# Performance work log

Measured on AMD Instinct MI355X. Metric: run time of the kernel, lower is better.

## Reference

```python
import jax, jax.numpy as jnp
import numpy as np

HEADS = 8
DIM_HEAD = 64
GROUPS = 32  # min(dim//4, 32) with dim=256
EPS = 1e-5

def setup_inputs() -> dict:
    key = jax.random.key(0)
    ks = jax.random.split(key, 5)
    C, H, W = 256, 256, 256
    hidden = HEADS * DIM_HEAD  # 512
    x = jax.random.normal(ks[0], (C, H, W), dtype=jnp.float32)
    gn_w = jnp.ones((C,), dtype=jnp.float32)
    gn_b = jnp.zeros((C,), dtype=jnp.float32)
    qkv_w = jax.random.normal(ks[1], (3 * hidden, C), dtype=jnp.float32) * (1.0 / np.sqrt(C))
    qkv_b = jax.random.normal(ks[2], (3 * hidden,), dtype=jnp.float32) * 0.02
    out_w = jax.random.normal(ks[3], (C, hidden), dtype=jnp.float32) * (1.0 / np.sqrt(hidden))
    out_b = jax.random.normal(ks[4], (C,), dtype=jnp.float32) * 0.02
    return {"x": x, "gn_w": gn_w, "gn_b": gn_b, "qkv_w": qkv_w,
            "qkv_b": qkv_b, "out_w": out_w, "out_b": out_b}

def reference(x, gn_w, gn_b, qkv_w, qkv_b, out_w, out_b):
    C, H, W = x.shape
    n = H * W
    # GroupNorm over (channels-in-group, h, w)
    xg = x.reshape(GROUPS, C // GROUPS, H, W)
    mean = xg.mean(axis=(1, 2, 3), keepdims=True)
    var = xg.var(axis=(1, 2, 3), keepdims=True)
    xn = ((xg - mean) * jax.lax.rsqrt(var + EPS)).reshape(C, H, W)
    xn = xn * gn_w[:, None, None] + gn_b[:, None, None]
    # 1x1 conv QKV projection
    qkv = jnp.einsum('oc,chw->ohw', qkv_w, xn) + qkv_b[:, None, None]
    # split as '(qkv heads c) h w -> qkv heads c (h w)'
    q, k, v = qkv.reshape(3, HEADS, DIM_HEAD, n)
    k = jax.nn.softmax(k, axis=-1)  # softmax over spatial axis
    context = jnp.einsum('hdn,hen->hde', k, v)   # [heads, d, d] small
    out = jnp.einsum('hde,hdn->hen', context, q)  # [heads, d, n]
    out = out.reshape(HEADS * DIM_HEAD, H, W)
    # 1x1 conv output projection
    return jnp.einsum('oc,chw->ohw', out_w, out) + out_b[:, None, None]
```

## Files before the change

kernel.cpp:

```cpp
#include <hip/hip_runtime.h>
#include <stdint.h>

typedef __attribute__((ext_vector_type(8))) short bf16x8;
typedef __attribute__((ext_vector_type(4))) float f32x4;
typedef __attribute__((ext_vector_type(4))) unsigned int u32x4;

#define NSP 65536

#define WS_XN     0ULL
#define WS_WFRAG  33554432ULL
#define WS_WEFRAG 34078720ULL
#define WS_PART   34209792ULL
#define WS_AB     34211840ULL
#define WS_CTX    34215936ULL
#define WS_W2     34347008ULL
#define WS_WEFF   35395584ULL
#define WS_BEFF   35657728ULL


__device__ __forceinline__ unsigned short f2bf(float f) {
  union { float f; uint32_t u; } v; v.f = f;
  uint32_t r = v.u + 0x7FFFu + ((v.u >> 16) & 1u);
  return (unsigned short)(r >> 16);
}
__device__ __forceinline__ float bf2f(unsigned short b) {
  union { uint32_t u; float f; } v; v.u = ((uint32_t)b) << 16;
  return v.f;
}

__global__ void k_stats(const float* __restrict__ x, float* __restrict__ part) {
  __shared__ float ss[256], sq[256];
  const int t = threadIdx.x, b = blockIdx.x;
  const f32x4* p = (const f32x4*)(x + (size_t)b * 65536);
  float s = 0.f, qq = 0.f;
  for (int k = 0; k < 64; ++k) {
    f32x4 v = __builtin_nontemporal_load(p + t + 256 * k);
    s  += v[0] + v[1] + v[2] + v[3];
    qq += v[0] * v[0] + v[1] * v[1] + v[2] * v[2] + v[3] * v[3];
  }
  ss[t] = s; sq[t] = qq;
  __syncthreads();
  for (int st = 128; st > 0; st >>= 1) {
    if (t < st) { ss[t] += ss[t + st]; sq[t] += sq[t + st]; }
    __syncthreads();
  }
  if (t == 0) { part[2 * b] = ss[0]; part[2 * b + 1] = sq[0]; }
}

__global__ void k_coef(const float* __restrict__ part, const float* __restrict__ gn_w,
                       const float* __restrict__ gn_b, float* __restrict__ ab) {
  const int c = threadIdx.x;
  const int g = c >> 3;
  float s = 0.f, q = 0.f;
  for (int j = 0; j < 8; ++j) { s += part[(g * 8 + j) * 2]; q += part[(g * 8 + j) * 2 + 1]; }
  const float inv = 1.0f / 524288.0f;
  const float mean = s * inv;
  const float var = q * inv - mean * mean;
  const float rstd = rsqrtf(var + 1e-5f);
  const float a = gn_w[c] * rstd;
  ab[c] = a;
  ab[256 + c] = gn_b[c] - mean * a;
}

__global__ void k_xn(const float* __restrict__ x, const float* __restrict__ ab,
                     unsigned short* __restrict__ xnf) {
  __shared__ float tile[64][66];
  const int t = threadIdx.x;
  const int nb = blockIdx.x, cb = blockIdx.y;
  {
    const int cl = t >> 2, nc = t & 3;
    const int c = cb * 64 + cl;
    const float a = ab[c], b = ab[256 + c];
    const f32x4* src = (const f32x4*)(x + (size_t)c * NSP + nb * 64 + nc * 16);
#pragma unroll
    for (int j = 0; j < 4; ++j) {
      f32x4 v = __builtin_nontemporal_load(src + j);
      v = v * a + b;
      *(f32x4*)&tile[cl][nc * 16 + j * 4] = v;
    }
  }
  __syncthreads();
  {
    const int l = t & 63, w0 = t >> 6;
    u32x4* xnf4 = (u32x4*)xnf;
#pragma unroll
    for (int u2 = 0; u2 < 2; ++u2) {
      const int fp = w0 + u2 * 4;
      const int fl = fp >> 1, ksl = fp & 1;
      union { unsigned short s[8]; u32x4 v; } pk2;
#pragma unroll
      for (int e = 0; e < 8; ++e)
        pk2.s[e] = f2bf(tile[ksl * 32 + (l >> 4) * 8 + e][fl * 16 + (l & 15)]);
      xnf4[((size_t)(nb * 4 + fl) * 8 + cb * 2 + ksl) * 64 + l] = pk2.v;
    }
  }
}

__global__ void k_wfrag(const float* __restrict__ qkv_w, unsigned short* __restrict__ wf) {
  const int blk = blockIdx.x;
  const int l = threadIdx.x;
  const int row = 512 + (blk & 63) * 16 + (l & 15);
  const int c0 = (blk >> 6) * 32 + (l >> 4) * 8;
  const float* src = qkv_w + (size_t)row * 256 + c0;
  union { unsigned short s[8]; u32x4 v; } u;
#pragma unroll
  for (int j = 0; j < 8; ++j) u.s[j] = f2bf(src[j]);
  *(u32x4*)(wf + ((size_t)blk * 64 + l) * 8) = u.v;
}

__launch_bounds__(512, 1)
__global__ void k_kvctx(const unsigned short* __restrict__ xnf,
                        const unsigned short* __restrict__ wfrag,
                        const float* __restrict__ qkv_b,
                        float* __restrict__ sump, float* __restrict__ ctxp) {
  __shared__ __align__(16) char lds[133120];
  const int t = threadIdx.x;
  const int w = t >> 6, l = t & 63;
  const int q = l & 15;
  const int h = blockIdx.x >> 5;
  const int chunk = blockIdx.x & 31;

  {
    const u32x4* wsrc = (const u32x4*)wfrag;
    u32x4* wdst = (u32x4*)lds;
#pragma unroll
    for (int r = 0; r < 8; ++r) {
      const int e = r * 512 + t;
      const int entry = e >> 6, l2 = e & 63;
      const int ph = entry >> 5, ks = (entry >> 2) & 7, jj = entry & 3;
      wdst[e] = wsrc[((size_t)(ks * 64 + ph * 32 + h * 4 + jj)) * 64 + l2];
    }
  }

  const f32x4 fz = {0.f, 0.f, 0.f, 0.f};
  f32x4 ctxa[4][4];
#pragma unroll
  for (int a = 0; a < 4; ++a)
#pragma unroll
    for (int b = 0; b < 4; ++b) ctxa[a][b] = fz;
  float srow[4] = {0.f, 0.f, 0.f, 0.f};
  float bk[4], bv[4];
#pragma unroll
  for (int jj = 0; jj < 4; ++jj) {
    bk[jj] = qkv_b[512 + h * 64 + jj * 16 + q];
    bv[jj] = qkv_b[1024 + h * 64 + jj * 16 + q];
  }

  const u32x4* xnf4 = (const u32x4*)xnf;
  u32x4* xa4 = (u32x4*)(lds + 65536);

  for (int st = 0; st < 8; ++st) {
    const size_t rg0 = (size_t)chunk * 128 + st * 16;
    __syncthreads();
#pragma unroll
    for (int r = 0; r < 8; ++r)
      xa4[r * 512 + t] = xnf4[rg0 * 512 + r * 512 + t];
    __syncthreads();
    const u32x4* gB = xnf4 + (rg0 + 8 + w) * 512 + l;

    f32x4 ak[2][4] = {{fz, fz, fz, fz}, {fz, fz, fz, fz}};
#pragma unroll
    for (int ks = 0; ks < 8; ++ks) {
      const bf16x8 xaA = *(const bf16x8*)(lds + 65536 + ((w * 8 + ks) * 64 + l) * 16);
      const bf16x8 xaB = *(const bf16x8*)(gB + ks * 64);
#pragma unroll
      for (int jj = 0; jj < 4; ++jj) {
        const bf16x8 bwk = *(const bf16x8*)(lds + ((ks * 4 + jj) * 64 + l) * 16);
        ak[0][jj] = __builtin_amdgcn_mfma_f32_16x16x32_bf16(xaA, bwk, ak[0][jj], 0, 0, 0);
        ak[1][jj] = __builtin_amdgcn_mfma_f32_16x16x32_bf16(xaB, bwk, ak[1][jj], 0, 0, 0);
      }
    }
    bf16x8 pk[4];
#pragma unroll
    for (int jj = 0; jj < 4; ++jj) {
      float s = 0.f;
      bf16x8 p;
#pragma unroll
      for (int r = 0; r < 4; ++r) {
        const unsigned short u0 = f2bf(__expf(ak[0][jj][r] + bk[jj]));
        const unsigned short u1 = f2bf(__expf(ak[1][jj][r] + bk[jj]));
        p[r] = (short)u0; p[r + 4] = (short)u1;
        s += bf2f(u0) + bf2f(u1);
      }
      pk[jj] = p;
      srow[jj] += s;
    }

    f32x4 av[2][4] = {{fz, fz, fz, fz}, {fz, fz, fz, fz}};
#pragma unroll
    for (int ks = 0; ks < 8; ++ks) {
      const bf16x8 xaA = *(const bf16x8*)(lds + 65536 + ((w * 8 + ks) * 64 + l) * 16);
      const bf16x8 xaB = *(const bf16x8*)(gB + ks * 64);
#pragma unroll
      for (int jj = 0; jj < 4; ++jj) {
        const bf16x8 bwv = *(const bf16x8*)(lds + (((8 + ks) * 4 + jj) * 64 + l) * 16);
        av[0][jj] = __builtin_amdgcn_mfma_f32_16x16x32_bf16(xaA, bwv, av[0][jj], 0, 0, 0);
        av[1][jj] = __builtin_amdgcn_mfma_f32_16x16x32_bf16(xaB, bwv, av[1][jj], 0, 0, 0);
      }
    }
    bf16x8 pv[4];
#pragma unroll
    for (int jj = 0; jj < 4; ++jj) {
      bf16x8 p;
#pragma unroll
      for (int r = 0; r < 4; ++r) {
        p[r]     = (short)f2bf(av[0][jj][r] + bv[jj]);
        p[r + 4] = (short)f2bf(av[1][jj][r] + bv[jj]);
      }
      pv[jj] = p;
    }

#pragma unroll
    for (int ja = 0; ja < 4; ++ja)
#pragma unroll
      for (int jb = 0; jb < 4; ++jb)
        ctxa[ja][jb] = __builtin_amdgcn_mfma_f32_16x16x32_bf16(pk[ja], pv[jb], ctxa[ja][jb], 0, 0, 0);
  }

  __syncthreads();
  {
    float* dw = (float*)lds + w * 4096 + l * 4;
#pragma unroll
    for (int ja = 0; ja < 4; ++ja)
#pragma unroll
      for (int jb = 0; jb < 4; ++jb)
        *(f32x4*)(dw + (ja * 4 + jb) * 256) = ctxa[ja][jb];
  }
  {
    float* srl = (float*)(lds + 131072);
#pragma unroll
    for (int jj = 0; jj < 4; ++jj) {
      float s = srow[jj];
      s += __shfl_xor(s, 16, 64);
      s += __shfl_xor(s, 32, 64);
      if (l < 16) srl[w * 64 + jj * 16 + q] = s;
    }
  }
  __syncthreads();
  {
    const float* dump = (const float*)lds;
    const f32x4 fz2 = {0.f, 0.f, 0.f, 0.f};
#pragma unroll
    for (int j = 0; j < 2; ++j) {
      const int m4 = j * 512 + t;
      f32x4 s = fz2;
#pragma unroll
      for (int w8 = 0; w8 < 8; ++w8)
        s += *(const f32x4*)(dump + w8 * 4096 + m4 * 4);
      *(f32x4*)(ctxp + ((size_t)(h * 32 + chunk) * 1024 + m4) * 4) = s;
    }
    if (t < 64) {
      const float* srl = (const float*)(lds + 131072);
      float s = 0.f;
#pragma unroll
      for (int w8 = 0; w8 < 8; ++w8) s += srl[w8 * 64 + t];
      sump[(size_t)(h * 64 + t) * 32 + chunk] = s;
    }
  }
}

__global__ void k_ctxred(const float* __restrict__ ctxp, const float* __restrict__ sump,
                         float* __restrict__ ctx, float* __restrict__ sexp) {
  const int t = threadIdx.x;
  if (blockIdx.x < 64) {
    const int m4 = blockIdx.x * 128 + t;
    const int h = m4 >> 10, p4 = m4 & 1023;
    f32x4 s = {0.f, 0.f, 0.f, 0.f};
#pragma unroll 8
    for (int c = 0; c < 32; ++c)
      s += *(const f32x4*)(ctxp + (((size_t)h * 32 + c) * 1024 + p4) * 4);
    const int jajb = p4 >> 6, ll = p4 & 63;
    const int ja = jajb >> 2, jb = jajb & 3;
    const int gg = ll >> 4, qq = ll & 15;
    float* cw = ctx + ((size_t)h * 64 + ja * 16 + gg * 4) * 64 + jb * 16 + qq;
    cw[0] = s[0]; cw[64] = s[1]; cw[128] = s[2]; cw[192] = s[3];
  } else {
    const int r = (blockIdx.x - 64) * 128 + t;
    float s = 0.f;
#pragma unroll 8
    for (int c = 0; c < 32; ++c) s += sump[(size_t)r * 32 + c];
    sexp[r] = s;
  }
}

__global__ void k_w2(const float* __restrict__ out_w, const float* __restrict__ ctx,
                     const float* __restrict__ sexp, float* __restrict__ w2) {
  const int r = blockIdx.x;
  const int h = r >> 6, d = r & 63;
  __shared__ float row[64];
  __shared__ float sinv;
  const int t = threadIdx.x;
  if (t < 64) row[t] = ctx[((size_t)h * 64 + d) * 64 + t];
  if (t == 0) sinv = 1.0f / sexp[r];
  __syncthreads();
  float a = 0.f;
  const float* wp = out_w + (size_t)t * 512 + h * 64;
#pragma unroll 8
  for (int e = 0; e < 64; ++e) a += wp[e] * row[e];
  w2[(size_t)t * 512 + r] = a * sinv;
}

__global__ void k_weff(const float* __restrict__ w2, const float* __restrict__ qkv_w,
                       const float* __restrict__ qkv_b, const float* __restrict__ out_b,
                       float* __restrict__ weff, float* __restrict__ beff) {
  const int o = blockIdx.x;
  const int c = threadIdx.x;
  __shared__ float row[512];
  __shared__ float red[256];
  row[c] = w2[(size_t)o * 512 + c];
  row[256 + c] = w2[(size_t)o * 512 + 256 + c];
  __syncthreads();
  float a = 0.f;
#pragma unroll 8
  for (int r = 0; r < 512; ++r) a += row[r] * qkv_w[(size_t)r * 256 + c];
  weff[o * 256 + c] = a;
  red[c] = row[c] * qkv_b[c] + row[256 + c] * qkv_b[256 + c];
  __syncthreads();
  for (int st = 128; st > 0; st >>= 1) {
    if (c < st) red[c] += red[c + st];
    __syncthreads();
  }
  if (c == 0) beff[o] = out_b[o] + red[0];
}

__global__ void k_wefrag(const float* __restrict__ weff, unsigned short* __restrict__ wf) {
  const int blk = blockIdx.x;
  const int l = threadIdx.x;
  const int row = (blk & 15) * 16 + (l & 15);
  const int c0 = (blk >> 4) * 32 + (l >> 4) * 8;
  const float* src = weff + (size_t)row * 256 + c0;
  union { unsigned short s[8]; u32x4 v; } u;
#pragma unroll
  for (int j = 0; j < 8; ++j) u.s[j] = f2bf(src[j]);
  *(u32x4*)(wf + ((size_t)blk * 64 + l) * 8) = u.v;
}

__launch_bounds__(256, 2)
__global__ void k_final(const unsigned short* __restrict__ xnf,
                        const unsigned short* __restrict__ wef,
                        const float* __restrict__ beff,
                        float* __restrict__ out) {
  __shared__ unsigned short xlds[32768];
  const int t = threadIdx.x;
  const int w = t >> 6, l = t & 63;
  const int q = l & 15, g = l >> 4;
  const int si = w >> 1, sj = w & 1;
  const size_t n0 = (size_t)blockIdx.x * 128;
  {
    const u32x4* gs = (const u32x4*)xnf + (size_t)blockIdx.x * 4096;
    u32x4* ld = (u32x4*)xlds;
#pragma unroll
    for (int k2 = 0; k2 < 16; ++k2)
      ld[t + 256 * k2] = gs[t + 256 * k2];
  }
  __syncthreads();
  const f32x4 fz = {0.f, 0.f, 0.f, 0.f};
  f32x4 acc[4][8];
#pragma unroll
  for (int i = 0; i < 4; ++i)
#pragma unroll
    for (int j = 0; j < 8; ++j) acc[i][j] = fz;
#pragma unroll
  for (int ks = 0; ks < 8; ++ks) {
    bf16x8 xa[4];
#pragma unroll
    for (int i = 0; i < 4; ++i)
      xa[i] = *(const bf16x8*)((const char*)xlds + (((si * 4 + i) * 8 + ks) * 64 + l) * 16);
#pragma unroll
    for (int jj = 0; jj < 8; ++jj) {
      const bf16x8 bw = *(const bf16x8*)(wef + (((size_t)(ks * 16 + sj * 8 + jj)) * 64 + l) * 8);
#pragma unroll
      for (int i = 0; i < 4; ++i)
        acc[i][jj] = __builtin_amdgcn_mfma_f32_16x16x32_bf16(xa[i], bw, acc[i][jj], 0, 0, 0);
    }
  }
  __syncthreads();
  float* trf = (float*)xlds;
#pragma unroll
  for (int k4 = 0; k4 < 4; ++k4) {
    if ((k4 >> 1) == sj) {
#pragma unroll
      for (int jj2 = 0; jj2 < 4; ++jj2) {
        const int jj = (k4 & 1) * 4 + jj2;
        const float be = beff[sj * 128 + jj * 16 + q];
#pragma unroll
        for (int i = 0; i < 4; ++i)
#pragma unroll
          for (int r = 0; r < 4; ++r)
            trf[(jj2 * 16 + q) * 129 + si * 64 + i * 16 + g * 4 + r] = acc[i][jj][r] + be;
      }
    }
    __syncthreads();
#pragma unroll
    for (int j = 0; j < 32; ++j) {
      const int mm = j * 256 + t;
      const int ol = mm >> 7, cc = mm & 127;
      out[(size_t)(k4 * 64 + ol) * NSP + n0 + cc] = trf[ol * 129 + cc];
    }
    __syncthreads();
  }
}

extern "C" void kernel_launch(void* const* d_in, const int* in_sizes, int n_in,
                              void* d_out, int out_size, void* d_ws, size_t ws_size,
                              hipStream_t stream) {
  const float* x     = (const float*)d_in[0];
  const float* gn_w  = (const float*)d_in[1];
  const float* gn_b  = (const float*)d_in[2];
  const float* qkv_w = (const float*)d_in[3];
  const float* qkv_b = (const float*)d_in[4];
  const float* out_w = (const float*)d_in[5];
  const float* out_b = (const float*)d_in[6];
  char* ws = (char*)d_ws;
  unsigned short* xnf = (unsigned short*)(ws + WS_XN);
  unsigned short* wf  = (unsigned short*)(ws + WS_WFRAG);
  unsigned short* wef = (unsigned short*)(ws + WS_WEFRAG);
  float* part   = (float*)(ws + WS_PART);
  float* ab     = (float*)(ws + WS_AB);
  float* ctx    = (float*)(ws + WS_CTX);
  float* w2     = (float*)(ws + WS_W2);
  float* weff   = (float*)(ws + WS_WEFF);
  float* beff   = (float*)(ws + WS_BEFF);
  float* out    = (float*)d_out;
  float* ctxp = (float*)((char*)d_out + 33554432ULL);
  float* sump = (float*)((char*)d_out + 37748736ULL);

  k_wfrag<<<512, 64, 0, stream>>>(qkv_w, wf);
  k_stats<<<256, 256, 0, stream>>>(x, part);
  k_coef<<<1, 256, 0, stream>>>(part, gn_w, gn_b, ab);
  k_xn<<<dim3(1024, 4), 256, 0, stream>>>(x, ab, xnf);
  k_kvctx<<<256, 512, 0, stream>>>(xnf, wf, qkv_b, sump, ctxp);
  k_ctxred<<<68, 128, 0, stream>>>(ctxp, sump, ctx, part);
  k_w2<<<512, 256, 0, stream>>>(out_w, ctx, part, w2);
  k_weff<<<256, 256, 0, stream>>>(w2, qkv_w, qkv_b, out_b, weff, beff);
  k_wefrag<<<128, 64, 0, stream>>>(weff, wef);
  k_final<<<512, 256, 0, stream>>>(xnf, wef, beff, out);
}
```

Measured before the change: 172.2 us.

## Split kvctx over more chunks, drop LDS staging of x, halve reduction LDS

Doubles the kvctx grid to 512 blocks (64 spatial chunks per head, each half as long). The A operand is now read straight from global memory instead of being staged through LDS, and the cross-wave context reduction runs in two passes of four waves each. Together these cut LDS from about 130KB to about 66KB, and launch bounds are relaxed to allow higher occupancy. In exchange there are more partial results for k_ctxred to sum, plus extra global loads and barriers.

```diff
diff --git a/kernel.cpp b/kernel.cpp
--- a/kernel.cpp
+++ b/kernel.cpp
@@ -108,17 +108,17 @@
   *(u32x4*)(wf + ((size_t)blk * 64 + l) * 8) = u.v;
 }
 
-__launch_bounds__(512, 1)
+__launch_bounds__(512, 4)
 __global__ void k_kvctx(const unsigned short* __restrict__ xnf,
                         const unsigned short* __restrict__ wfrag,
                         const float* __restrict__ qkv_b,
                         float* __restrict__ sump, float* __restrict__ ctxp) {
-  __shared__ __align__(16) char lds[133120];
+  __shared__ __align__(16) char lds[67584];
   const int t = threadIdx.x;
   const int w = t >> 6, l = t & 63;
   const int q = l & 15;
-  const int h = blockIdx.x >> 5;
-  const int chunk = blockIdx.x & 31;
+  const int h = blockIdx.x >> 6;
+  const int chunk = blockIdx.x & 63;
 
   {
     const u32x4* wsrc = (const u32x4*)wfrag;
@@ -131,6 +131,7 @@
       wdst[e] = wsrc[((size_t)(ks * 64 + ph * 32 + h * 4 + jj)) * 64 + l2];
     }
   }
+  __syncthreads();
 
   const f32x4 fz = {0.f, 0.f, 0.f, 0.f};
   f32x4 ctxa[4][4];
@@ -147,21 +148,16 @@
   }
 
   const u32x4* xnf4 = (const u32x4*)xnf;
-  u32x4* xa4 = (u32x4*)(lds + 65536);
-
-  for (int st = 0; st < 8; ++st) {
-    const size_t rg0 = (size_t)chunk * 128 + st * 16;
-    __syncthreads();
-#pragma unroll
-    for (int r = 0; r < 8; ++r)
-      xa4[r * 512 + t] = xnf4[rg0 * 512 + r * 512 + t];
-    __syncthreads();
+
+  for (int st = 0; st < 4; ++st) {
+    const size_t rg0 = (size_t)chunk * 64 + st * 16;
+    const u32x4* gA = xnf4 + (rg0 + w) * 512 + l;
     const u32x4* gB = xnf4 + (rg0 + 8 + w) * 512 + l;
 
     f32x4 ak[2][4] = {{fz, fz, fz, fz}, {fz, fz, fz, fz}};
 #pragma unroll
     for (int ks = 0; ks < 8; ++ks) {
-      const bf16x8 xaA = *(const bf16x8*)(lds + 65536 + ((w * 8 + ks) * 64 + l) * 16);
+      const bf16x8 xaA = *(const bf16x8*)(gA + ks * 64);
       const bf16x8 xaB = *(const bf16x8*)(gB + ks * 64);
 #pragma unroll
       for (int jj = 0; jj < 4; ++jj) {
@@ -189,7 +185,7 @@
     f32x4 av[2][4] = {{fz, fz, fz, fz}, {fz, fz, fz, fz}};
 #pragma unroll
     for (int ks = 0; ks < 8; ++ks) {
-      const bf16x8 xaA = *(const bf16x8*)(lds + 65536 + ((w * 8 + ks) * 64 + l) * 16);
+      const bf16x8 xaA = *(const bf16x8*)(gA + ks * 64);
       const bf16x8 xaB = *(const bf16x8*)(gB + ks * 64);
 #pragma unroll
       for (int jj = 0; jj < 4; ++jj) {
@@ -219,15 +215,7 @@
 
   __syncthreads();
   {
-    float* dw = (float*)lds + w * 4096 + l * 4;
-#pragma unroll
-    for (int ja = 0; ja < 4; ++ja)
-#pragma unroll
-      for (int jb = 0; jb < 4; ++jb)
-        *(f32x4*)(dw + (ja * 4 + jb) * 256) = ctxa[ja][jb];
-  }
-  {
-    float* srl = (float*)(lds + 131072);
+    float* srl = (float*)(lds + 65536);
 #pragma unroll
     for (int jj = 0; jj < 4; ++jj) {
       float s = srow[jj];
@@ -236,25 +224,50 @@
       if (l < 16) srl[w * 64 + jj * 16 + q] = s;
     }
   }
-  __syncthreads();
+  if (w < 4) {
+    float* dw = (float*)lds + w * 4096 + l * 4;
+#pragma unroll
+    for (int ja = 0; ja < 4; ++ja)
+#pragma unroll
+      for (int jb = 0; jb < 4; ++jb)
+        *(f32x4*)(dw + (ja * 4 + jb) * 256) = ctxa[ja][jb];
+  }
+  __syncthreads();
+  f32x4 part0 = fz, part1 = fz;
   {
     const float* dump = (const float*)lds;
-    const f32x4 fz2 = {0.f, 0.f, 0.f, 0.f};
-#pragma unroll
-    for (int j = 0; j < 2; ++j) {
-      const int m4 = j * 512 + t;
-      f32x4 s = fz2;
-#pragma unroll
-      for (int w8 = 0; w8 < 8; ++w8)
-        s += *(const f32x4*)(dump + w8 * 4096 + m4 * 4);
-      *(f32x4*)(ctxp + ((size_t)(h * 32 + chunk) * 1024 + m4) * 4) = s;
-    }
+#pragma unroll
+    for (int w4 = 0; w4 < 4; ++w4) {
+      part0 += *(const f32x4*)(dump + w4 * 4096 + t * 4);
+      part1 += *(const f32x4*)(dump + w4 * 4096 + (512 + t) * 4);
+    }
+  }
+  __syncthreads();
+  if (w >= 4) {
+    float* dw = (float*)lds + (w - 4) * 4096 + l * 4;
+#pragma unroll
+    for (int ja = 0; ja < 4; ++ja)
+#pragma unroll
+      for (int jb = 0; jb < 4; ++jb)
+        *(f32x4*)(dw + (ja * 4 + jb) * 256) = ctxa[ja][jb];
+  }
+  __syncthreads();
+  {
+    const float* dump = (const float*)lds;
+#pragma unroll
+    for (int w4 = 0; w4 < 4; ++w4) {
+      part0 += *(const f32x4*)(dump + w4 * 4096 + t * 4);
+      part1 += *(const f32x4*)(dump + w4 * 4096 + (512 + t) * 4);
+    }
+    float* cp = ctxp + (size_t)blockIdx.x * 4096;
+    *(f32x4*)(cp + t * 4) = part0;
+    *(f32x4*)(cp + (512 + t) * 4) = part1;
     if (t < 64) {
-      const float* srl = (const float*)(lds + 131072);
+      const float* srl = (const float*)(lds + 65536);
       float s = 0.f;
 #pragma unroll
       for (int w8 = 0; w8 < 8; ++w8) s += srl[w8 * 64 + t];
-      sump[(size_t)(h * 64 + t) * 32 + chunk] = s;
+      sump[(size_t)(h * 64 + t) * 64 + chunk] = s;
     }
   }
 }
@@ -267,8 +280,8 @@
     const int h = m4 >> 10, p4 = m4 & 1023;
     f32x4 s = {0.f, 0.f, 0.f, 0.f};
 #pragma unroll 8
-    for (int c = 0; c < 32; ++c)
-      s += *(const f32x4*)(ctxp + (((size_t)h * 32 + c) * 1024 + p4) * 4);
+    for (int c = 0; c < 64; ++c)
+      s += *(const f32x4*)(ctxp + (((size_t)h * 64 + c) * 1024 + p4) * 4);
     const int jajb = p4 >> 6, ll = p4 & 63;
     const int ja = jajb >> 2, jb = jajb & 3;
     const int gg = ll >> 4, qq = ll & 15;
@@ -278,7 +291,7 @@
     const int r = (blockIdx.x - 64) * 128 + t;
     float s = 0.f;
 #pragma unroll 8
-    for (int c = 0; c < 32; ++c) s += sump[(size_t)r * 32 + c];
+    for (int c = 0; c < 64; ++c) s += sump[(size_t)r * 64 + c];
     sexp[r] = s;
   }
 }
@@ -423,13 +436,13 @@
   float* beff   = (float*)(ws + WS_BEFF);
   float* out    = (float*)d_out;
   float* ctxp = (float*)((char*)d_out + 33554432ULL);
-  float* sump = (float*)((char*)d_out + 37748736ULL);
+  float* sump = (float*)((char*)d_out + 41943040ULL);
 
   k_wfrag<<<512, 64, 0, stream>>>(qkv_w, wf);
   k_stats<<<256, 256, 0, stream>>>(x, part);
   k_coef<<<1, 256, 0, stream>>>(part, gn_w, gn_b, ab);
   k_xn<<<dim3(1024, 4), 256, 0, stream>>>(x, ab, xnf);
-  k_kvctx<<<256, 512, 0, stream>>>(xnf, wf, qkv_b, sump, ctxp);
+  k_kvctx<<<512, 512, 0, stream>>>(xnf, wf, qkv_b, sump, ctxp);
   k_ctxred<<<68, 128, 0, stream>>>(ctxp, sump, ctx, part);
   k_w2<<<512, 256, 0, stream>>>(out_w, ctx, part, w2);
   k_weff<<<256, 256, 0, stream>>>(w2, qkv_w, qkv_b, out_b, weff, beff);
```

Result: slower. 503.4 us (+192.3%).

## Double k_kvctx block to 1024 threads, one row-group per wave

Applied to the files above, without the earlier changes.

The K/V-context kernel now launches 16 waves per block instead of 8. Each wave handles one 16-row spatial tile instead of two: waves 0-7 read their tile from LDS and waves 8-15 read it from global memory. The aim is more waves in flight to hide MFMA and memory latency. In exchange, the weight fragments read from LDS and the per-wave context accumulators are doubled across waves, and the cross-wave reduction becomes a two-pass LDS sum with extra barriers. Register pressure per thread also tightens under the 1024-thread launch bound, and the zero-padded bf16 halves waste half of each context MFMA.

```diff
diff --git a/kernel.cpp b/kernel.cpp
--- a/kernel.cpp
+++ b/kernel.cpp
@@ -108,12 +108,12 @@
   *(u32x4*)(wf + ((size_t)blk * 64 + l) * 8) = u.v;
 }
 
-__launch_bounds__(512, 1)
+__launch_bounds__(1024, 1)
 __global__ void k_kvctx(const unsigned short* __restrict__ xnf,
                         const unsigned short* __restrict__ wfrag,
                         const float* __restrict__ qkv_b,
                         float* __restrict__ sump, float* __restrict__ ctxp) {
-  __shared__ __align__(16) char lds[133120];
+  __shared__ __align__(16) char lds[135168];
   const int t = threadIdx.x;
   const int w = t >> 6, l = t & 63;
   const int q = l & 15;
@@ -124,8 +124,8 @@
     const u32x4* wsrc = (const u32x4*)wfrag;
     u32x4* wdst = (u32x4*)lds;
 #pragma unroll
-    for (int r = 0; r < 8; ++r) {
-      const int e = r * 512 + t;
+    for (int r = 0; r < 4; ++r) {
+      const int e = r * 1024 + t;
       const int entry = e >> 6, l2 = e & 63;
       const int ph = entry >> 5, ks = (entry >> 2) & 7, jj = entry & 3;
       wdst[e] = wsrc[((size_t)(ks * 64 + ph * 32 + h * 4 + jj)) * 64 + l2];
@@ -149,83 +149,75 @@
   const u32x4* xnf4 = (const u32x4*)xnf;
   u32x4* xa4 = (u32x4*)(lds + 65536);
 
-  for (int st = 0; st < 8; ++st) {
-    const size_t rg0 = (size_t)chunk * 128 + st * 16;
-    __syncthreads();
-#pragma unroll
-    for (int r = 0; r < 8; ++r)
-      xa4[r * 512 + t] = xnf4[rg0 * 512 + r * 512 + t];
-    __syncthreads();
-    const u32x4* gB = xnf4 + (rg0 + 8 + w) * 512 + l;
-
-    f32x4 ak[2][4] = {{fz, fz, fz, fz}, {fz, fz, fz, fz}};
+  auto body = [&](auto xald) {
+    f32x4 ak[4] = {fz, fz, fz, fz};
 #pragma unroll
     for (int ks = 0; ks < 8; ++ks) {
-      const bf16x8 xaA = *(const bf16x8*)(lds + 65536 + ((w * 8 + ks) * 64 + l) * 16);
-      const bf16x8 xaB = *(const bf16x8*)(gB + ks * 64);
+      const bf16x8 xa = xald(ks);
 #pragma unroll
       for (int jj = 0; jj < 4; ++jj) {
         const bf16x8 bwk = *(const bf16x8*)(lds + ((ks * 4 + jj) * 64 + l) * 16);
-        ak[0][jj] = __builtin_amdgcn_mfma_f32_16x16x32_bf16(xaA, bwk, ak[0][jj], 0, 0, 0);
-        ak[1][jj] = __builtin_amdgcn_mfma_f32_16x16x32_bf16(xaB, bwk, ak[1][jj], 0, 0, 0);
+        ak[jj] = __builtin_amdgcn_mfma_f32_16x16x32_bf16(xa, bwk, ak[jj], 0, 0, 0);
       }
     }
     bf16x8 pk[4];
 #pragma unroll
     for (int jj = 0; jj < 4; ++jj) {
       float s = 0.f;
-      bf16x8 p;
+      bf16x8 p = {0, 0, 0, 0, 0, 0, 0, 0};
 #pragma unroll
       for (int r = 0; r < 4; ++r) {
-        const unsigned short u0 = f2bf(__expf(ak[0][jj][r] + bk[jj]));
-        const unsigned short u1 = f2bf(__expf(ak[1][jj][r] + bk[jj]));
-        p[r] = (short)u0; p[r + 4] = (short)u1;
-        s += bf2f(u0) + bf2f(u1);
+        const unsigned short u0 = f2bf(__expf(ak[jj][r] + bk[jj]));
+        p[r] = (short)u0;
+        s += bf2f(u0);
       }
       pk[jj] = p;
       srow[jj] += s;
     }
-
-    f32x4 av[2][4] = {{fz, fz, fz, fz}, {fz, fz, fz, fz}};
+    f32x4 av[4] = {fz, fz, fz, fz};
 #pragma unroll
     for (int ks = 0; ks < 8; ++ks) {
-      const bf16x8 xaA = *(const bf16x8*)(lds + 65536 + ((w * 8 + ks) * 64 + l) * 16);
-      const bf16x8 xaB = *(const bf16x8*)(gB + ks * 64);
+      const bf16x8 xa = xald(ks);
 #pragma unroll
       for (int jj = 0; jj < 4; ++jj) {
         const bf16x8 bwv = *(const bf16x8*)(lds + (((8 + ks) * 4 + jj) * 64 + l) * 16);
-        av[0][jj] = __builtin_amdgcn_mfma_f32_16x16x32_bf16(xaA, bwv, av[0][jj], 0, 0, 0);
-        av[1][jj] = __builtin_amdgcn_mfma_f32_16x16x32_bf16(xaB, bwv, av[1][jj], 0, 0, 0);
+        av[jj] = __builtin_amdgcn_mfma_f32_16x16x32_bf16(xa, bwv, av[jj], 0, 0, 0);
       }
     }
     bf16x8 pv[4];
 #pragma unroll
     for (int jj = 0; jj < 4; ++jj) {
-      bf16x8 p;
-#pragma unroll
-      for (int r = 0; r < 4; ++r) {
-        p[r]     = (short)f2bf(av[0][jj][r] + bv[jj]);
-        p[r + 4] = (short)f2bf(av[1][jj][r] + bv[jj]);
-      }
+      bf16x8 p = {0, 0, 0, 0, 0, 0, 0, 0};
+#pragma unroll
+      for (int r = 0; r < 4; ++r)
+        p[r] = (short)f2bf(av[jj][r] + bv[jj]);
       pv[jj] = p;
     }
-
 #pragma unroll
     for (int ja = 0; ja < 4; ++ja)
 #pragma unroll
       for (int jb = 0; jb < 4; ++jb)
         ctxa[ja][jb] = __builtin_amdgcn_mfma_f32_16x16x32_bf16(pk[ja], pv[jb], ctxa[ja][jb], 0, 0, 0);
-  }
-
-  __syncthreads();
-  {
-    float* dw = (float*)lds + w * 4096 + l * 4;
-#pragma unroll
-    for (int ja = 0; ja < 4; ++ja)
-#pragma unroll
-      for (int jb = 0; jb < 4; ++jb)
-        *(f32x4*)(dw + (ja * 4 + jb) * 256) = ctxa[ja][jb];
-  }
+  };
+
+  for (int st = 0; st < 8; ++st) {
+    const size_t rg0 = (size_t)chunk * 128 + st * 16;
+    __syncthreads();
+#pragma unroll
+    for (int r = 0; r < 4; ++r)
+      xa4[r * 1024 + t] = xnf4[rg0 * 512 + r * 1024 + t];
+    __syncthreads();
+
+    if (w < 8) {
+      const char* xbase = lds + 65536 + (w * 8 * 64 + l) * 16;
+      body([&](int ks) { return *(const bf16x8*)(xbase + ks * 1024); });
+    } else {
+      const u32x4* gX = xnf4 + (rg0 + w) * 512 + l;
+      body([&](int ks) { return *(const bf16x8*)(gX + ks * 64); });
+    }
+  }
+
+  __syncthreads();
   {
     float* srl = (float*)(lds + 131072);
 #pragma unroll
@@ -236,24 +228,43 @@
       if (l < 16) srl[w * 64 + jj * 16 + q] = s;
     }
   }
-  __syncthreads();
+  if (w < 8) {
+    float* dw = (float*)lds + w * 4096 + l * 4;
+#pragma unroll
+    for (int ja = 0; ja < 4; ++ja)
+#pragma unroll
+      for (int jb = 0; jb < 4; ++jb)
+        *(f32x4*)(dw + (ja * 4 + jb) * 256) = ctxa[ja][jb];
+  }
+  __syncthreads();
+  f32x4 part = fz;
   {
     const float* dump = (const float*)lds;
-    const f32x4 fz2 = {0.f, 0.f, 0.f, 0.f};
-#pragma unroll
-    for (int j = 0; j < 2; ++j) {
-      const int m4 = j * 512 + t;
-      f32x4 s = fz2;
-#pragma unroll
-      for (int w8 = 0; w8 < 8; ++w8)
-        s += *(const f32x4*)(dump + w8 * 4096 + m4 * 4);
-      *(f32x4*)(ctxp + ((size_t)(h * 32 + chunk) * 1024 + m4) * 4) = s;
-    }
+#pragma unroll
+    for (int w8 = 0; w8 < 8; ++w8)
+      part += *(const f32x4*)(dump + w8 * 4096 + t * 4);
+  }
+  __syncthreads();
+  if (w >= 8) {
+    float* dw = (float*)lds + (w - 8) * 4096 + l * 4;
+#pragma unroll
+    for (int ja = 0; ja < 4; ++ja)
+#pragma unroll
+      for (int jb = 0; jb < 4; ++jb)
+        *(f32x4*)(dw + (ja * 4 + jb) * 256) = ctxa[ja][jb];
+  }
+  __syncthreads();
+  {
+    const float* dump = (const float*)lds;
+#pragma unroll
+    for (int w8 = 0; w8 < 8; ++w8)
+      part += *(const f32x4*)(dump + w8 * 4096 + t * 4);
+    *(f32x4*)(ctxp + (size_t)blockIdx.x * 4096 + t * 4) = part;
     if (t < 64) {
       const float* srl = (const float*)(lds + 131072);
       float s = 0.f;
 #pragma unroll
-      for (int w8 = 0; w8 < 8; ++w8) s += srl[w8 * 64 + t];
+      for (int w8 = 0; w8 < 16; ++w8) s += srl[w8 * 64 + t];
       sump[(size_t)(h * 64 + t) * 32 + chunk] = s;
     }
   }
@@ -429,7 +440,7 @@
   k_stats<<<256, 256, 0, stream>>>(x, part);
   k_coef<<<1, 256, 0, stream>>>(part, gn_w, gn_b, ab);
   k_xn<<<dim3(1024, 4), 256, 0, stream>>>(x, ab, xnf);
-  k_kvctx<<<256, 512, 0, stream>>>(xnf, wf, qkv_b, sump, ctxp);
+  k_kvctx<<<256, 1024, 0, stream>>>(xnf, wf, qkv_b, sump, ctxp);
   k_ctxred<<<68, 128, 0, stream>>>(ctxp, sump, ctx, part);
   k_w2<<<512, 256, 0, stream>>>(out_w, ctx, part, w2);
   k_weff<<<256, 256, 0, stream>>>(w2, qkv_w, qkv_b, out_b, weff, beff);
```

Measured after the change: 220.4 us. 28.0% more time.

## Reassociate effective-weight product, fuse bf16 fragment packing, swizzle final block order

Applied to the files above, without the earlier changes.

The small weight-folding chain changes association order. It first computes G = ctx_norm^T · Wq per head (8 blocks), then out_w · G with bf16 fragment packing fused in (16 blocks), replacing three kernels (k_w2, k_weff, k_wefrag). This removes one launch and the intermediate weff round-trip, but the new kernels use very few blocks with long serial loops, so the work is less parallel. k_final also remaps block indices with a stride-8 swizzle, likely to spread blocks differently across XCDs and caches.

```diff
diff --git a/kernel.cpp b/kernel.cpp
--- a/kernel.cpp
+++ b/kernel.cpp
@@ -13,8 +13,8 @@
 #define WS_PART   34209792ULL
 #define WS_AB     34211840ULL
 #define WS_CTX    34215936ULL
-#define WS_W2     34347008ULL
-#define WS_WEFF   35395584ULL
+#define WS_G      34347008ULL
+#define WS_G2     34871296ULL
 #define WS_BEFF   35657728ULL
 
 
@@ -283,56 +283,80 @@
   }
 }
 
-__global__ void k_w2(const float* __restrict__ out_w, const float* __restrict__ ctx,
-                     const float* __restrict__ sexp, float* __restrict__ w2) {
-  const int r = blockIdx.x;
-  const int h = r >> 6, d = r & 63;
-  __shared__ float row[64];
-  __shared__ float sinv;
+__global__ void k_G(const float* __restrict__ ctx, const float* __restrict__ sexp,
+                    const float* __restrict__ qkv_w, const float* __restrict__ qkv_b,
+                    float* __restrict__ G, float* __restrict__ g2) {
+  __shared__ float cn[64][65];
+  __shared__ float sinv[64];
+  const int h = blockIdx.x, t = threadIdx.x;
+  if (t < 64) sinv[t] = 1.0f / sexp[h * 64 + t];
+  __syncthreads();
+#pragma unroll
+  for (int j = 0; j < 16; ++j) {
+    const int idx = j * 256 + t;
+    const int d = idx >> 6, e = idx & 63;
+    cn[d][e] = ctx[(size_t)h * 4096 + idx] * sinv[d];
+  }
+  __syncthreads();
+  const int c = t;
+  for (int e8 = 0; e8 < 8; ++e8) {
+    float acc[8] = {0.f, 0.f, 0.f, 0.f, 0.f, 0.f, 0.f, 0.f};
+    for (int d = 0; d < 64; ++d) {
+      const float wq = qkv_w[(size_t)(h * 64 + d) * 256 + c];
+#pragma unroll
+      for (int e = 0; e < 8; ++e) acc[e] += cn[d][e8 * 8 + e] * wq;
+    }
+#pragma unroll
+    for (int e = 0; e < 8; ++e)
+      G[(size_t)(h * 64 + e8 * 8 + e) * 256 + c] = acc[e];
+  }
+  if (t < 64) {
+    float s = 0.f;
+    for (int d = 0; d < 64; ++d) s += cn[d][t] * qkv_b[h * 64 + d];
+    g2[h * 64 + t] = s;
+  }
+}
+
+__global__ void k_weffrag(const float* __restrict__ out_w, const float* __restrict__ G,
+                          const float* __restrict__ g2, const float* __restrict__ out_b,
+                          unsigned short* __restrict__ wef, float* __restrict__ beff) {
+  __shared__ float ow[16][513];
+  __shared__ float wl[16][257];
+  const int ro = blockIdx.x;
   const int t = threadIdx.x;
-  if (t < 64) row[t] = ctx[((size_t)h * 64 + d) * 64 + t];
-  if (t == 0) sinv = 1.0f / sexp[r];
-  __syncthreads();
-  float a = 0.f;
-  const float* wp = out_w + (size_t)t * 512 + h * 64;
-#pragma unroll 8
-  for (int e = 0; e < 64; ++e) a += wp[e] * row[e];
-  w2[(size_t)t * 512 + r] = a * sinv;
-}
-
-__global__ void k_weff(const float* __restrict__ w2, const float* __restrict__ qkv_w,
-                       const float* __restrict__ qkv_b, const float* __restrict__ out_b,
-                       float* __restrict__ weff, float* __restrict__ beff) {
-  const int o = blockIdx.x;
-  const int c = threadIdx.x;
-  __shared__ float row[512];
-  __shared__ float red[256];
-  row[c] = w2[(size_t)o * 512 + c];
-  row[256 + c] = w2[(size_t)o * 512 + 256 + c];
-  __syncthreads();
-  float a = 0.f;
-#pragma unroll 8
-  for (int r = 0; r < 512; ++r) a += row[r] * qkv_w[(size_t)r * 256 + c];
-  weff[o * 256 + c] = a;
-  red[c] = row[c] * qkv_b[c] + row[256 + c] * qkv_b[256 + c];
-  __syncthreads();
-  for (int st = 128; st > 0; st >>= 1) {
-    if (c < st) red[c] += red[c + st];
-    __syncthreads();
-  }
-  if (c == 0) beff[o] = out_b[o] + red[0];
-}
-
-__global__ void k_wefrag(const float* __restrict__ weff, unsigned short* __restrict__ wf) {
-  const int blk = blockIdx.x;
-  const int l = threadIdx.x;
-  const int row = (blk & 15) * 16 + (l & 15);
-  const int c0 = (blk >> 4) * 32 + (l >> 4) * 8;
-  const float* src = weff + (size_t)row * 256 + c0;
-  union { unsigned short s[8]; u32x4 v; } u;
-#pragma unroll
-  for (int j = 0; j < 8; ++j) u.s[j] = f2bf(src[j]);
-  *(u32x4*)(wf + ((size_t)blk * 64 + l) * 8) = u.v;
+#pragma unroll
+  for (int j = 0; j < 32; ++j) {
+    const int idx = j * 256 + t;
+    ow[idx >> 9][idx & 511] = out_w[(size_t)(ro * 16 + (idx >> 9)) * 512 + (idx & 511)];
+  }
+  __syncthreads();
+  const int c = t;
+  float acc[16];
+#pragma unroll
+  for (int i = 0; i < 16; ++i) acc[i] = 0.f;
+  for (int he = 0; he < 512; ++he) {
+    const float gv = G[(size_t)he * 256 + c];
+#pragma unroll
+    for (int o16 = 0; o16 < 16; ++o16) acc[o16] += ow[o16][he] * gv;
+  }
+#pragma unroll
+  for (int o16 = 0; o16 < 16; ++o16) wl[o16][c] = acc[o16];
+  if (t < 16) {
+    float b = out_b[ro * 16 + t];
+    for (int he = 0; he < 512; ++he) b += ow[t][he] * g2[he];
+    beff[ro * 16 + t] = b;
+  }
+  __syncthreads();
+#pragma unroll
+  for (int it = 0; it < 2; ++it) {
+    const int idx = it * 256 + t;
+    const int ks = idx >> 6, l = idx & 63;
+    const int rloc = l & 15, c0 = ks * 32 + (l >> 4) * 8;
+    union { unsigned short s[8]; u32x4 v; } u;
+#pragma unroll
+    for (int j2 = 0; j2 < 8; ++j2) u.s[j2] = f2bf(wl[rloc][c0 + j2]);
+    *(u32x4*)(wef + ((size_t)(ks * 16 + ro) * 64 + l) * 8) = u.v;
+  }
 }
 
 __launch_bounds__(256, 2)
@@ -345,9 +369,10 @@
   const int w = t >> 6, l = t & 63;
   const int q = l & 15, g = l >> 4;
   const int si = w >> 1, sj = w & 1;
-  const size_t n0 = (size_t)blockIdx.x * 128;
-  {
-    const u32x4* gs = (const u32x4*)xnf + (size_t)blockIdx.x * 4096;
+  const int bid = (blockIdx.x & 7) * 64 + (blockIdx.x >> 3);
+  const size_t n0 = (size_t)bid * 128;
+  {
+    const u32x4* gs = (const u32x4*)xnf + (size_t)bid * 4096;
     u32x4* ld = (u32x4*)xlds;
 #pragma unroll
     for (int k2 = 0; k2 < 16; ++k2)
@@ -418,8 +443,8 @@
   float* part   = (float*)(ws + WS_PART);
   float* ab     = (float*)(ws + WS_AB);
   float* ctx    = (float*)(ws + WS_CTX);
-  float* w2     = (float*)(ws + WS_W2);
-  float* weff   = (float*)(ws + WS_WEFF);
+  float* G      = (float*)(ws + WS_G);
+  float* g2     = (float*)(ws + WS_G2);
   float* beff   = (float*)(ws + WS_BEFF);
   float* out    = (float*)d_out;
   float* ctxp = (float*)((char*)d_out + 33554432ULL);
@@ -431,8 +456,7 @@
   k_xn<<<dim3(1024, 4), 256, 0, stream>>>(x, ab, xnf);
   k_kvctx<<<256, 512, 0, stream>>>(xnf, wf, qkv_b, sump, ctxp);
   k_ctxred<<<68, 128, 0, stream>>>(ctxp, sump, ctx, part);
-  k_w2<<<512, 256, 0, stream>>>(out_w, ctx, part, w2);
-  k_weff<<<256, 256, 0, stream>>>(w2, qkv_w, qkv_b, out_b, weff, beff);
-  k_wefrag<<<128, 64, 0, stream>>>(weff, wef);
+  k_G<<<8, 256, 0, stream>>>(ctx, part, qkv_w, qkv_b, G, g2);
+  k_weffrag<<<16, 256, 0, stream>>>(out_w, G, g2, out_b, wef, beff);
   k_final<<<512, 256, 0, stream>>>(xnf, wef, beff, out);
 }
```

Result: slower. 237.1 us (+37.7%).
